# Optimization experiments

Measured on AMD Instinct MI355X. Metric: run time of the kernel, lower is better.

## Reference

```python
import jax, jax.numpy as jnp
import numpy as np

L, S, R, NUM_RESNET = 6, 2, 3, 3
N = 2 ** L            # 64 blocks per axis
NX = N * S            # 128 grid points per axis
NCART_SIDE = 80
NCART = NCART_SIDE ** 2


def _perm_idx(L_, l):
    delta = 2 ** (L_ - l - 1)
    t = np.tile(np.arange(2) * delta, delta) + np.repeat(np.arange(delta), 2)
    t = np.tile(t, 2 ** l) + np.repeat(np.arange(2 ** l) * 2 ** (L_ - l), 2 ** (L_ - l))
    return jnp.asarray(t)


def _switch_idx(L_):
    h = L_ // 2
    t = np.tile(np.arange(2 ** h) * 2 ** h, 2 ** h) + np.repeat(np.arange(2 ** h), 2 ** h)
    return jnp.asarray(t)


def _bmm2(x, g_left, g_right):
    # x: (B,p,i,q,j). Right block-diag GEMM on (q,j), then left block-diag GEMM on (p,i).
    y = jnp.einsum('bpiqj,qjk->bpiqk', x, g_right)
    return jnp.einsum('bpiqk,pio->bpoqk', y, g_left)


def _complex_layer(xr, xi, p):
    # p: stacked (r1,i1,r2,i2,r3,i3,r4,i4); complex-style cross products of the original.
    r1, i1, r2, i2, r3, i3, r4, i4 = p
    yr = _bmm2(xr, r1, r1) + _bmm2(xr, i1, i1) + _bmm2(xi, r2, i2) + _bmm2(xi, i2, r2)
    yi = _bmm2(xi, r3, r3) + _bmm2(xi, i3, i3) + _bmm2(xr, r4, i4) + _bmm2(xr, i4, r4)
    return yr, yi


def _u_layer(xr, xi, p):
    ur1, ui1, ur2, ui2, ur3, ui3, ur4, ui4 = p
    return (_bmm2(xr, ur1, ur1) + _bmm2(xr, ui2, ui2)
            + _bmm2(xi, ur3, ui3) + _bmm2(xi, ui4, ur4))


def _permute(yr, yi, idx):
    yr = jnp.take(jnp.take(yr, idx, axis=1), idx, axis=3)
    yi = jnp.take(jnp.take(yi, idx, axis=1), idx, axis=3)
    return yr, yi


def _merge(y):  # (B,N,R,N,R) -> (B,N/2,2R,N/2,2R)
    return y.reshape(y.shape[0], N // 2, 2 * R, N // 2, 2 * R)


def _split(y):  # inverse of _merge
    return y.reshape(y.shape[0], N, R, N, R)


def reference(x, Vp, Hp, Mp, Gp, Up, cart_mat, r_index):
    B = x.shape[0]
    xr = x[..., 0].reshape(B, N, S, N, S)
    xi = x[..., 1].reshape(B, N, S, N, S)
    yr, yi = _complex_layer(xr, xi, Vp)                       # (B,N,R,N,R)
    for li, l in enumerate(range(L - 1, L // 2 - 1, -1)):     # H stages (permute then merge-GEMM)
        yr, yi = _permute(yr, yi, _perm_idx(L, l))
        yr, yi = _complex_layer(_merge(yr), _merge(yi), Hp[li])
        yr, yi = _split(yr), _split(yi)
    yr, yi = _permute(yr, yi, _switch_idx(L))                 # middle switch shuffle
    for k in range(NUM_RESNET):                               # residual M blocks
        zr, zi = _complex_layer(yr, yi, Mp[k])
        yr, yi = yr + zr, yi + zi
    for li, l in enumerate(range(L // 2 - 1, -1, -1)):        # G stages (merge-GEMM then permute)
        yr, yi = _complex_layer(_merge(yr), _merge(yi), Gp[li])
        yr, yi = _split(yr), _split(yi)
        yr, yi = _permute(yr, yi, _perm_idx(L, l))
    y = _u_layer(yr, yi, Up).reshape(B, NX * NX)              # real output, (B,NX,NX) flattened
    y = jnp.take(y, r_index, axis=1)                          # polar reindexing
    out = y @ cart_mat.T                                      # polar -> cartesian interpolation
    return out.reshape(B, NCART_SIDE, NCART_SIDE)


def setup_inputs() -> dict:
    key = jax.random.key(0)
    ks = jax.random.split(key, 9)
    B = 128
    x = jax.random.normal(ks[0], (B, NX, NX, 2), dtype=jnp.float32)
    Vp = jax.random.normal(ks[1], (8, N, S, R), dtype=jnp.float32) * 0.35
    Hp = jax.random.normal(ks[2], (L // 2, 8, N // 2, 2 * R, 2 * R), dtype=jnp.float32) * 0.2
    Mp = jax.random.normal(ks[3], (NUM_RESNET, 8, N, R, R), dtype=jnp.float32) * 0.25
    Gp = jax.random.normal(ks[4], (L // 2, 8, N // 2, 2 * R, 2 * R), dtype=jnp.float32) * 0.2
    Up = jax.random.normal(ks[5], (8, N, R, S), dtype=jnp.float32) * 0.35
    cart_mat = jax.random.normal(ks[6], (NCART, NX * NX), dtype=jnp.float32) * 0.01
    r_index = jax.random.permutation(ks[7], NX * NX).astype(jnp.int32)
    return {"x": x, "Vp": Vp, "Hp": Hp, "Mp": Mp, "Gp": Gp, "Up": Up,
            "cart_mat": cart_mat, "r_index": r_index}
```

## Files before the change

### kernel.cpp

```cpp
#include <hip/hip_runtime.h>


typedef _Float16 f16;
typedef __attribute__((ext_vector_type(8))) short sx8;
typedef __attribute__((ext_vector_type(4))) float fx4;
typedef __attribute__((ext_vector_type(8))) unsigned short usx8;
typedef __attribute__((ext_vector_type(4))) unsigned short usx4;

__device__ __forceinline__ unsigned short f2bf(float f) {
  unsigned u = __builtin_bit_cast(unsigned, f);
  u = (u + 0x7FFFu + ((u >> 16) & 1u)) >> 16;
  return (unsigned short)u;
}
__device__ __forceinline__ float bf2f(unsigned short h) {
  return __builtin_bit_cast(float, ((unsigned)h) << 16);
}

template<int ID>
__device__ __forceinline__ int rp_apply(int k) {
  if constexpr (ID == 0) { return k; }
  else if constexpr (ID == 3) { return (k & 7) * 8 + (k >> 3); }
  else {
    constexpr int l = (ID == 1) ? 4 : (ID == 2) ? 3 : (ID == 4) ? 2 : (ID == 5) ? 1 : 0;
    constexpr int d = 1 << (5 - l);
    constexpr int m2 = 2 * d;
    int g = k / m2, r = k % m2;
    return g * m2 + (r & 1) * d + (r >> 1);
  }
}

__device__ __forceinline__ void term_decode(int t, int& lm, int& rm,
                                            bool& useXi, bool& toYi) {
  lm = (t < 2) ? t : (t < 4) ? (t + 4) : (t - 2);
  rm = (t >= 2 && t <= 5) ? (lm ^ 1) : lm;
  useXi = (t >= 4);
  toYi = (t >> 1) & 1;
}

#define SMEM_BYTES 36864

__device__ __forceinline__ void layer6(int g, int b, int P, int Q,
                                       const float* __restrict__ wp,
                                       const f16* ldsX, float* Y0, float* Y1,
                                       f16* __restrict__ yr,
                                       f16* __restrict__ yi) {
  int lm0, rm0, lm1, rm1;
  switch (g) {
    case 0:  lm0 = 0; rm0 = 0; lm1 = 1; rm1 = 1; break;
    case 1:  lm0 = 6; rm0 = 7; lm1 = 7; rm1 = 6; break;
    case 2:  lm0 = 2; rm0 = 3; lm1 = 3; rm1 = 2; break;
    default: lm0 = 4; rm0 = 4; lm1 = 5; rm1 = 5; break;
  }
  const int xbase = (g & 2) ? 36 : 0;
  float X[36], Y[36];
#pragma unroll
  for (int k = 0; k < 36; ++k) X[k] = (float)ldsX[(xbase + k) * 128 + b];
#pragma unroll
  for (int k = 0; k < 36; ++k) Y[k] = 0.f;

  for (int tt = 0; tt < 2; ++tt) {
    const int lm = tt ? lm1 : lm0;
    const int rm = tt ? rm1 : rm0;
    const float* Lw = wp + ((size_t)lm * 32 + P) * 36;
    const float* Rw = wp + ((size_t)rm * 32 + Q) * 36;
#pragma unroll
    for (int i = 0; i < 6; ++i) {
      float tk[6] = {0.f, 0.f, 0.f, 0.f, 0.f, 0.f};
#pragma unroll
      for (int j = 0; j < 6; ++j) {
        float xv = X[i * 6 + j];
#pragma unroll
        for (int k = 0; k < 6; ++k) tk[k] += xv * Rw[j * 6 + k];
      }
#pragma unroll
      for (int o = 0; o < 6; ++o) {
        float lv = Lw[i * 6 + o];
#pragma unroll
        for (int k = 0; k < 6; ++k) Y[o * 6 + k] += lv * tk[k];
      }
    }
  }
  __syncthreads();
  if (g == 2) {
#pragma unroll
    for (int k = 0; k < 36; ++k) Y0[k * 128 + b] = Y[k];
  } else if (g == 3) {
#pragma unroll
    for (int k = 0; k < 36; ++k) Y1[k * 128 + b] = Y[k];
  }
  __syncthreads();
  if (g == 0) {
#pragma unroll
    for (int k = 0; k < 36; ++k) {
      float v = Y[k] + Y0[k * 128 + b];
      yr[((size_t)((P * 6 + k / 6) * 192 + Q * 6 + k % 6)) * 128 + b] = (f16)v;
    }
  } else if (g == 1) {
#pragma unroll
    for (int k = 0; k < 36; ++k) {
      float v = Y[k] + Y1[k * 128 + b];
      yi[((size_t)((P * 6 + k / 6) * 192 + Q * 6 + k % 6)) * 128 + b] = (f16)v;
    }
  }
}

__global__ __launch_bounds__(256) void k_transpose(const float* __restrict__ x,
                                                   f16* __restrict__ xtr,
                                                   f16* __restrict__ xti) {
  __shared__ float ls[2][32][129];
  const int t = threadIdx.x;
  const int u = blockIdx.x;
  const int v0 = blockIdx.y * 32;
  for (int it = 0; it < 32; ++it) {
    int b = it * 4 + (t >> 6);
    int r = t & 63;
    int v = r >> 1, ch = r & 1;
    ls[ch][v][b] = x[(((size_t)b * 128 + u) * 128 + (v0 + v)) * 2 + ch];
  }
  __syncthreads();
  for (int it = 0; it < 32; ++it) {
    int idx = it * 256 + t;
    int ch = idx >> 12;
    int v = (idx >> 7) & 31;
    int b = idx & 127;
    f16* dst = ch ? xti : xtr;
    dst[((size_t)(u * 128 + v0 + v)) * 128 + b] = (f16)ls[ch][v][b];
  }
}

__global__ __launch_bounds__(512, 4) void k_vh(const f16* __restrict__ xtr,
                                               const f16* __restrict__ xti,
                                               f16* __restrict__ yr,
                                               f16* __restrict__ yi,
                                               const float* __restrict__ vp,
                                               const float* __restrict__ hp) {
  __shared__ __align__(16) char smem[SMEM_BYTES];
  f16* ldsX = (f16*)smem;
  float* Y0 = (float*)smem;
  float* Y1 = (float*)(smem + 18432);
  const int t = threadIdx.x;
  const int P = blockIdx.x, Q = blockIdx.y;
  const int g = __builtin_amdgcn_readfirstlane(t >> 7);
  const int b = t & 127;

  const int pp = g >> 1, qq = g & 1;
  const int p = 2 * P + pp, q = 2 * Q + qq;
  float Xr[4], Xi[4];
#pragma unroll
  for (int i = 0; i < 2; ++i)
#pragma unroll
    for (int j = 0; j < 2; ++j) {
      size_t off = ((size_t)((4 * P + 2 * pp + i) * 128 + (4 * Q + 2 * qq + j))) * 128 + b;
      Xr[i * 2 + j] = (float)xtr[off];
      Xi[i * 2 + j] = (float)xti[off];
    }
  float Ar[9], Ai[9];
#pragma unroll
  for (int k = 0; k < 9; ++k) { Ar[k] = 0.f; Ai[k] = 0.f; }
  for (int tt = 0; tt < 8; ++tt) {
    int lm, rm; bool useXi, toYi;
    term_decode(tt, lm, rm, useXi, toYi);
    const float* Lw = vp + ((size_t)lm * 64 + p) * 6;
    const float* Rw = vp + ((size_t)rm * 64 + q) * 6;
#pragma unroll
    for (int i = 0; i < 2; ++i) {
      float x0, x1;
      if (useXi) { x0 = Xi[i * 2 + 0]; x1 = Xi[i * 2 + 1]; }
      else       { x0 = Xr[i * 2 + 0]; x1 = Xr[i * 2 + 1]; }
      float t0 = x0 * Rw[0] + x1 * Rw[3];
      float t1 = x0 * Rw[1] + x1 * Rw[4];
      float t2 = x0 * Rw[2] + x1 * Rw[5];
      if (toYi) {
#pragma unroll
        for (int o = 0; o < 3; ++o) {
          float lv = Lw[i * 3 + o];
          Ai[o*3+0] += lv * t0; Ai[o*3+1] += lv * t1; Ai[o*3+2] += lv * t2;
        }
      } else {
#pragma unroll
        for (int o = 0; o < 3; ++o) {
          float lv = Lw[i * 3 + o];
          Ar[o*3+0] += lv * t0; Ar[o*3+1] += lv * t1; Ar[o*3+2] += lv * t2;
        }
      }
    }
  }
#pragma unroll
  for (int o = 0; o < 3; ++o)
#pragma unroll
    for (int k = 0; k < 3; ++k) {
      int ch = (3 * pp + o) * 6 + (3 * qq + k);
      ldsX[ch * 128 + b] = (f16)Ar[o * 3 + k];
      ldsX[(36 + ch) * 128 + b] = (f16)Ai[o * 3 + k];
    }
  __syncthreads();
  layer6(g, b, P, Q, hp, ldsX, Y0, Y1, yr, yi);
}

template<int PERM>
__global__ __launch_bounds__(512, 4) void k_hg(const f16* __restrict__ xr,
                                               const f16* __restrict__ xi,
                                               f16* __restrict__ yr,
                                               f16* __restrict__ yi,
                                               const float* __restrict__ wp) {
  __shared__ __align__(16) char smem[SMEM_BYTES];
  f16* ldsX = (f16*)smem;
  float* Y0 = (float*)smem;
  float* Y1 = (float*)(smem + 18432);
  const int t = threadIdx.x;
  const int P = blockIdx.x, Q = blockIdx.y;

  for (int r = 0; r < 3; ++r) {
    int idx = t + r * 512;
    if (idx < 1152) {
      int c = idx >> 4, o8 = (idx & 15) * 8;
      int cc = (c < 36) ? c : c - 36;
      int I = cc / 6, J = cc % 6;
      int grow = rp_apply<PERM>(2 * P + I / 3) * 3 + I % 3;
      int gcol = rp_apply<PERM>(2 * Q + J / 3) * 3 + J % 3;
      const f16* src = (c < 36) ? xr : xi;
      usx8 v = *(const usx8*)(src + ((size_t)(grow * 192 + gcol)) * 128 + o8);
      *(usx8*)(ldsX + c * 128 + o8) = v;
    }
  }
  __syncthreads();
  const int g = __builtin_amdgcn_readfirstlane(t >> 7);
  const int b = t & 127;
  layer6(g, b, P, Q, wp, ldsX, Y0, Y1, yr, yi);
}

__global__ __launch_bounds__(512, 4) void k_mg(const f16* __restrict__ xr,
                                               const f16* __restrict__ xi,
                                               f16* __restrict__ yr,
                                               f16* __restrict__ yi,
                                               const float* __restrict__ mp,
                                               const float* __restrict__ gp) {
  __shared__ __align__(16) char smem[SMEM_BYTES];
  f16* ldsX = (f16*)smem;
  float* Y0 = (float*)smem;
  float* Y1 = (float*)(smem + 18432);
  const int t = threadIdx.x;
  const int P = blockIdx.x, Q = blockIdx.y;
  const int g = __builtin_amdgcn_readfirstlane(t >> 7);
  const int b = t & 127;

  const int aa = g >> 1, bb = g & 1;
  const int p = 2 * P + aa, q = 2 * Q + bb;
  const int prow = rp_apply<3>(p) * 3, pcol = rp_apply<3>(q) * 3;
  float Xr[9], Xi[9];
#pragma unroll
  for (int i = 0; i < 3; ++i)
#pragma unroll
    for (int j = 0; j < 3; ++j) {
      size_t off = ((size_t)((prow + i) * 192 + (pcol + j))) * 128 + b;
      Xr[i * 3 + j] = (float)xr[off];
      Xi[i * 3 + j] = (float)xi[off];
    }
  for (int lk = 0; lk < 3; ++lk) {
    const float* wp = mp + (size_t)lk * (8 * 64 * 9);
    float Yr9[9], Yi9[9];
#pragma unroll
    for (int k = 0; k < 9; ++k) { Yr9[k] = Xr[k]; Yi9[k] = Xi[k]; }
    for (int tt = 0; tt < 8; ++tt) {
      int lm, rm; bool useXi, toYi;
      term_decode(tt, lm, rm, useXi, toYi);
      const float* Lw = wp + ((size_t)lm * 64 + p) * 9;
      const float* Rw = wp + ((size_t)rm * 64 + q) * 9;
#pragma unroll
      for (int i = 0; i < 3; ++i) {
        float x0, x1, x2;
        if (useXi) { x0 = Xi[i*3+0]; x1 = Xi[i*3+1]; x2 = Xi[i*3+2]; }
        else       { x0 = Xr[i*3+0]; x1 = Xr[i*3+1]; x2 = Xr[i*3+2]; }
        float t0 = x0 * Rw[0] + x1 * Rw[3] + x2 * Rw[6];
        float t1 = x0 * Rw[1] + x1 * Rw[4] + x2 * Rw[7];
        float t2 = x0 * Rw[2] + x1 * Rw[5] + x2 * Rw[8];
        if (toYi) {
#pragma unroll
          for (int o = 0; o < 3; ++o) {
            float lv = Lw[i * 3 + o];
            Yi9[o*3+0] += lv * t0; Yi9[o*3+1] += lv * t1; Yi9[o*3+2] += lv * t2;
          }
        } else {
#pragma unroll
          for (int o = 0; o < 3; ++o) {
            float lv = Lw[i * 3 + o];
            Yr9[o*3+0] += lv * t0; Yr9[o*3+1] += lv * t1; Yr9[o*3+2] += lv * t2;
          }
        }
      }
    }
#pragma unroll
    for (int k = 0; k < 9; ++k) { Xr[k] = Yr9[k]; Xi[k] = Yi9[k]; }
  }
#pragma unroll
  for (int i = 0; i < 3; ++i)
#pragma unroll
    for (int j = 0; j < 3; ++j) {
      int ch = (3 * aa + i) * 6 + (3 * bb + j);
      ldsX[ch * 128 + b] = (f16)Xr[i * 3 + j];
      ldsX[(36 + ch) * 128 + b] = (f16)Xi[i * 3 + j];
    }
  __syncthreads();
  layer6(g, b, P, Q, gp, ldsX, Y0, Y1, yr, yi);
}

__global__ __launch_bounds__(128, 2) void k_u(const f16* __restrict__ xr,
                                              const f16* __restrict__ xi,
                                              unsigned short* __restrict__ ut,
                                              const float* __restrict__ wp) {
  const int b = threadIdx.x;
  const int p = blockIdx.x, q = blockIdx.y;
  int rrow[3], rcol[3];
#pragma unroll
  for (int i = 0; i < 3; ++i) {
    rrow[i] = rp_apply<6>(p) * 3 + i;
    rcol[i] = rp_apply<6>(q) * 3 + i;
  }
  float X[9], Y[4] = {0.f, 0.f, 0.f, 0.f};
  auto loadX = [&](const f16* src) {
#pragma unroll
    for (int i = 0; i < 3; ++i)
#pragma unroll
      for (int j = 0; j < 3; ++j)
        X[i * 3 + j] = (float)src[((size_t)(rrow[i] * 192 + rcol[j])) * 128 + b];
  };
  auto term = [&](int lm, int rm) {
    const float* Lw = wp + ((size_t)lm * 64 + p) * 6;
    const float* Rw = wp + ((size_t)rm * 64 + q) * 6;
#pragma unroll
    for (int i = 0; i < 3; ++i) {
      float t0 = X[i*3+0] * Rw[0] + X[i*3+1] * Rw[2] + X[i*3+2] * Rw[4];
      float t1 = X[i*3+0] * Rw[1] + X[i*3+1] * Rw[3] + X[i*3+2] * Rw[5];
      Y[0] += Lw[i*2+0] * t0; Y[1] += Lw[i*2+0] * t1;
      Y[2] += Lw[i*2+1] * t0; Y[3] += Lw[i*2+1] * t1;
    }
  };
  loadX(xr); term(0, 0); term(3, 3);
  loadX(xi); term(4, 5); term(7, 6);
#pragma unroll
  for (int o = 0; o < 2; ++o)
#pragma unroll
    for (int k = 0; k < 2; ++k)
      ut[((size_t)((p * 2 + o) * 128 + (q * 2 + k))) * 128 + b] = f2bf(Y[o * 2 + k]);
}

__global__ __launch_bounds__(256) void k_gather(const unsigned short* __restrict__ ut,
                                                const int* __restrict__ r_index,
                                                unsigned short* __restrict__ yg) {
  __shared__ unsigned short ls[64][130];
  __shared__ int ridx[64];
  const int t = threadIdx.x;
  const int m0 = blockIdx.x * 64;
  if (t < 64) ridx[t] = r_index[m0 + t];
  __syncthreads();
  for (int it = 0; it < 32; ++it) {
    int idx = it * 256 + t;
    int ml = idx >> 7, b = idx & 127;
    ls[ml][b] = ut[(size_t)ridx[ml] * 128 + b];
  }
  __syncthreads();
  int b = t >> 1, half = t & 1;
#pragma unroll
  for (int c = 0; c < 4; ++c) {
    usx8 v;
#pragma unroll
    for (int e = 0; e < 8; ++e) v[e] = ls[half * 32 + c * 8 + e][b];
    *(usx8*)(yg + (size_t)b * 16384 + m0 + half * 32 + c * 8) = v;
  }
}

#define G2_KC 8
#define G2_STEPS 32
#define G2_PITCH 72

__global__ __launch_bounds__(256) void k_gemm2(const unsigned short* __restrict__ yg,
                                               const float* __restrict__ cart,
                                               unsigned short* __restrict__ partial) {
  __shared__ unsigned short As[2][128][G2_PITCH];
  __shared__ unsigned short Bs[2][64][G2_PITCH];
  const int t = threadIdx.x;
  const int lane = t & 63, w = t >> 6;
  const int kc = blockIdx.x;
  const int c0 = blockIdx.y * 64;
  const int k0 = kc * 2048;

  fx4 acc[2][4];
#pragma unroll
  for (int i = 0; i < 2; ++i)
#pragma unroll
    for (int j = 0; j < 4; ++j) acc[i][j] = (fx4)0.f;

  auto ldA = [&](int rep, int kpos) -> usx8 {
    int c = t + rep * 256;
    return *(const usx8*)(yg + (size_t)(c >> 3) * 16384 + kpos + (c & 7) * 8);
  };
  auto stA = [&](int buf, int rep, usx8 v) {
    int c = t + rep * 256;
    *(usx8*)(&As[buf][c >> 3][(c & 7) * 8]) = v;
  };
  auto ldB = [&](int rep, int kpos, fx4* f0, fx4* f1) {
    int c = t + rep * 256;
    const float* p = cart + (size_t)(c0 + (c >> 3)) * 16384 + kpos + (c & 7) * 8;
    *f0 = *(const fx4*)p;
    *f1 = *(const fx4*)(p + 4);
  };
  auto stB = [&](int buf, int rep, fx4 f0, fx4 f1) {
    int c = t + rep * 256;
    usx8 v;
    v[0]=f2bf(f0[0]); v[1]=f2bf(f0[1]); v[2]=f2bf(f0[2]); v[3]=f2bf(f0[3]);
    v[4]=f2bf(f1[0]); v[5]=f2bf(f1[1]); v[6]=f2bf(f1[2]); v[7]=f2bf(f1[3]);
    *(usx8*)(&Bs[buf][c >> 3][(c & 7) * 8]) = v;
  };

  {
    usx8 a0 = ldA(0, k0), a1 = ldA(1, k0), a2 = ldA(2, k0), a3 = ldA(3, k0);
    fx4 b00, b01, b10, b11;
    ldB(0, k0, &b00, &b01); ldB(1, k0, &b10, &b11);
    stA(0, 0, a0); stA(0, 1, a1); stA(0, 2, a2); stA(0, 3, a3);
    stB(0, 0, b00, b01); stB(0, 1, b10, b11);
  }
  __syncthreads();

  for (int s = 0; s < G2_STEPS; ++s) {
    const int cur = s & 1;
    usx8 av[4]; fx4 b00, b01, b10, b11;
    const bool pf = (s + 1 < G2_STEPS);
    if (pf) {
      int kpos = k0 + (s + 1) * 64;
      av[0] = ldA(0, kpos); av[1] = ldA(1, kpos);
      av[2] = ldA(2, kpos); av[3] = ldA(3, kpos);
      ldB(0, kpos, &b00, &b01); ldB(1, kpos, &b10, &b11);
    }
    sx8 af[2][2], bf[4][2];
#pragma unroll
    for (int mi = 0; mi < 2; ++mi)
#pragma unroll
      for (int kk = 0; kk < 2; ++kk)
        af[mi][kk] = *(const sx8*)(&As[cur][w * 32 + mi * 16 + (lane & 15)][kk * 32 + (lane >> 4) * 8]);
#pragma unroll
    for (int ni = 0; ni < 4; ++ni)
#pragma unroll
      for (int kk = 0; kk < 2; ++kk)
        bf[ni][kk] = *(const sx8*)(&Bs[cur][ni * 16 + (lane & 15)][kk * 32 + (lane >> 4) * 8]);
#pragma unroll
    for (int kk = 0; kk < 2; ++kk)
#pragma unroll
      for (int mi = 0; mi < 2; ++mi)
#pragma unroll
        for (int ni = 0; ni < 4; ++ni)
          acc[mi][ni] = __builtin_amdgcn_mfma_f32_16x16x32_bf16(af[mi][kk], bf[ni][kk], acc[mi][ni], 0, 0, 0);
    if (pf) {
      stA(cur ^ 1, 0, av[0]); stA(cur ^ 1, 1, av[1]);
      stA(cur ^ 1, 2, av[2]); stA(cur ^ 1, 3, av[3]);
      stB(cur ^ 1, 0, b00, b01); stB(cur ^ 1, 1, b10, b11);
    }
    __syncthreads();
  }

#pragma unroll
  for (int mi = 0; mi < 2; ++mi) {
    int brow = w * 32 + mi * 16 + (lane >> 4) * 4;
#pragma unroll
    for (int ni = 0; ni < 4; ++ni) {
      int cc = c0 + ni * 16 + (lane & 15);
#pragma unroll
      for (int r = 0; r < 4; ++r)
        partial[((size_t)kc * 128 + brow + r) * 6400 + cc] = f2bf(acc[mi][ni][r]);
    }
  }
}

__global__ __launch_bounds__(256) void k_reduce2(const unsigned short* __restrict__ partial,
                                                 float* __restrict__ out) {
  int i = blockIdx.x * 256 + threadIdx.x;
  fx4 s = (fx4)0.f;
#pragma unroll
  for (int kc = 0; kc < G2_KC; ++kc) {
    usx4 v = *(const usx4*)(partial + (size_t)kc * 819200 + (size_t)i * 4);
    s[0] += bf2f(v[0]); s[1] += bf2f(v[1]); s[2] += bf2f(v[2]); s[3] += bf2f(v[3]);
  }
  *(fx4*)(out + (size_t)i * 4) = s;
}

extern "C" void kernel_launch(void* const* d_in, const int* in_sizes, int n_in,
                              void* d_out, int out_size, void* d_ws, size_t ws_size,
                              hipStream_t stream) {
  const float* x    = (const float*)d_in[0];
  const float* Vp   = (const float*)d_in[1];
  const float* Hp   = (const float*)d_in[2];
  const float* Mp   = (const float*)d_in[3];
  const float* Gp   = (const float*)d_in[4];
  const float* Up   = (const float*)d_in[5];
  const float* cart = (const float*)d_in[6];
  const int*   ridx = (const int*)d_in[7];
  float* out = (float*)d_out;
  unsigned short* hb = (unsigned short*)d_ws;

  const size_t PSZ = 4718592;
  f16* P0r = (f16*)(hb);
  f16* P0i = (f16*)(hb + PSZ);
  f16* P1r = (f16*)(hb + 2 * PSZ);
  f16* P1i = (f16*)(hb + 3 * PSZ);
  f16* xtr = (f16*)(hb + 4 * PSZ);
  f16* xti = (f16*)(hb + 4 * PSZ + 2097152);
  unsigned short* ut = hb + 4 * PSZ;
  unsigned short* yg = hb + 4 * PSZ + 2097152;
  unsigned short* partial = hb;

  const size_t HSZ = 8 * 32 * 36;

  k_transpose<<<dim3(128, 4), 256, 0, stream>>>(x, xtr, xti);
  k_vh<<<dim3(32, 32), 512, 0, stream>>>(xtr, xti, P0r, P0i, Vp, Hp + 0 * HSZ);
  k_hg<1><<<dim3(32, 32), 512, 0, stream>>>(P0r, P0i, P1r, P1i, Hp + 1 * HSZ);
  k_hg<2><<<dim3(32, 32), 512, 0, stream>>>(P1r, P1i, P0r, P0i, Hp + 2 * HSZ);
  k_mg<<<dim3(32, 32), 512, 0, stream>>>(P0r, P0i, P1r, P1i, Mp, Gp + 0 * HSZ);
  k_hg<4><<<dim3(32, 32), 512, 0, stream>>>(P1r, P1i, P0r, P0i, Gp + 1 * HSZ);
  k_hg<5><<<dim3(32, 32), 512, 0, stream>>>(P0r, P0i, P1r, P1i, Gp + 2 * HSZ);
  k_u<<<dim3(64, 64), 128, 0, stream>>>(P1r, P1i, ut, Up);
  k_gather<<<dim3(256), 256, 0, stream>>>(ut, ridx, yg);
  k_gemm2<<<dim3(G2_KC, 100), 256, 0, stream>>>(yg, cart, partial);
  k_reduce2<<<dim3(800), 256, 0, stream>>>(partial, out);
  (void)in_sizes; (void)n_in; (void)out_size; (void)ws_size;
}
```

Measured before the change: 300.1 us.

## Recast butterfly layers as per-block dense 72x72 operators applied with MFMA

Each H/G layer block is rewritten so the Kronecker-product weights (left and right, complex cross terms) are expanded in LDS into a dense 72x72 fp16 operator. That operator is then applied to the 72x128 batch tile with 16x16x32 f16 MFMA instructions instead of scalar FMA loops. The V layer and the three M resnet layers are also folded algebraically into the following H or G operator, so each fused kernel does one MFMA GEMM. The cost is building dense operators per block and extra fp16 rounding of the combined weights.

```diff
diff --git a/kernel.cpp b/kernel.cpp
--- a/kernel.cpp
+++ b/kernel.cpp
@@ -2,6 +2,7 @@
 
 
 typedef _Float16 f16;
+typedef __attribute__((ext_vector_type(8))) _Float16 hx8;
 typedef __attribute__((ext_vector_type(8))) short sx8;
 typedef __attribute__((ext_vector_type(4))) float fx4;
 typedef __attribute__((ext_vector_type(8))) unsigned short usx8;
@@ -29,79 +30,58 @@
   }
 }
 
-__device__ __forceinline__ void term_decode(int t, int& lm, int& rm,
-                                            bool& useXi, bool& toYi) {
-  lm = (t < 2) ? t : (t < 4) ? (t + 4) : (t - 2);
-  rm = (t >= 2 && t <= 5) ? (lm ^ 1) : lm;
-  useXi = (t >= 4);
-  toYi = (t >> 1) & 1;
-}
-
-#define SMEM_BYTES 36864
-
-__device__ __forceinline__ void layer6(int g, int b, int P, int Q,
-                                       const float* __restrict__ wp,
-                                       const f16* ldsX, float* Y0, float* Y1,
-                                       f16* __restrict__ yr,
-                                       f16* __restrict__ yi) {
-  int lm0, rm0, lm1, rm1;
-  switch (g) {
-    case 0:  lm0 = 0; rm0 = 0; lm1 = 1; rm1 = 1; break;
-    case 1:  lm0 = 6; rm0 = 7; lm1 = 7; rm1 = 6; break;
-    case 2:  lm0 = 2; rm0 = 3; lm1 = 3; rm1 = 2; break;
-    default: lm0 = 4; rm0 = 4; lm1 = 5; rm1 = 5; break;
-  }
-  const int xbase = (g & 2) ? 36 : 0;
-  float X[36], Y[36];
-#pragma unroll
-  for (int k = 0; k < 36; ++k) X[k] = (float)ldsX[(xbase + k) * 128 + b];
-#pragma unroll
-  for (int k = 0; k < 36; ++k) Y[k] = 0.f;
-
-  for (int tt = 0; tt < 2; ++tt) {
-    const int lm = tt ? lm1 : lm0;
-    const int rm = tt ? rm1 : rm0;
-    const float* Lw = wp + ((size_t)lm * 32 + P) * 36;
-    const float* Rw = wp + ((size_t)rm * 32 + Q) * 36;
-#pragma unroll
-    for (int i = 0; i < 6; ++i) {
-      float tk[6] = {0.f, 0.f, 0.f, 0.f, 0.f, 0.f};
-#pragma unroll
-      for (int j = 0; j < 6; ++j) {
-        float xv = X[i * 6 + j];
-#pragma unroll
-        for (int k = 0; k < 6; ++k) tk[k] += xv * Rw[j * 6 + k];
+__device__ __forceinline__ void qterm(int co, int ci, int tt, int& lm, int& rm) {
+  if (!co && !ci) { lm = tt;     rm = tt;     }
+  else if (!co)   { lm = 2 + tt; rm = 3 - tt; }
+  else if (!ci)   { lm = 6 + tt; rm = 7 - tt; }
+  else            { lm = 4 + tt; rm = 4 + tt; }
+}
+
+template<int NKC, int GP>
+__device__ __forceinline__ void lay_mfma(const f16* Gl, const f16* Xl,
+                                         int P, int Q, int t,
+                                         f16* __restrict__ yr,
+                                         f16* __restrict__ yi) {
+  const int w = t >> 6, lane = t & 63;
+  const int lrow = lane & 15, lgr = lane >> 4;
+  fx4 acc[5][2];
+#pragma unroll
+  for (int mt = 0; mt < 5; ++mt) { acc[mt][0] = (fx4)0.f; acc[mt][1] = (fx4)0.f; }
+#pragma unroll
+  for (int kc = 0; kc < NKC; ++kc) {
+    hx8 af[5], bf[2];
+#pragma unroll
+    for (int mt = 0; mt < 5; ++mt)
+      af[mt] = *(const hx8*)(Gl + (mt * 16 + lrow) * GP + kc * 32 + lgr * 8);
+#pragma unroll
+    for (int nt2 = 0; nt2 < 2; ++nt2) {
+      int n = (2 * w + nt2) * 16 + lrow;
+      int k0 = kc * 32 + lgr * 8;
+      hx8 b;
+#pragma unroll
+      for (int j = 0; j < 8; ++j) b[j] = Xl[(k0 + j) * 136 + n];
+      bf[nt2] = b;
+    }
+#pragma unroll
+    for (int mt = 0; mt < 5; ++mt)
+#pragma unroll
+      for (int nt2 = 0; nt2 < 2; ++nt2)
+        acc[mt][nt2] = __builtin_amdgcn_mfma_f32_16x16x32_f16(af[mt], bf[nt2], acc[mt][nt2], 0, 0, 0);
+  }
+#pragma unroll
+  for (int mt = 0; mt < 5; ++mt)
+#pragma unroll
+    for (int nt2 = 0; nt2 < 2; ++nt2)
+#pragma unroll
+      for (int r = 0; r < 4; ++r) {
+        int row = mt * 16 + lgr * 4 + r;
+        if (row >= 72) continue;
+        int n = (2 * w + nt2) * 16 + lrow;
+        int c = row >= 36;
+        int s = row - c * 36;
+        size_t off = ((size_t)((P * 6 + s / 6) * 192 + (Q * 6 + s % 6))) * 128 + n;
+        (c ? yi : yr)[off] = (f16)acc[mt][nt2][r];
       }
-#pragma unroll
-      for (int o = 0; o < 6; ++o) {
-        float lv = Lw[i * 6 + o];
-#pragma unroll
-        for (int k = 0; k < 6; ++k) Y[o * 6 + k] += lv * tk[k];
-      }
-    }
-  }
-  __syncthreads();
-  if (g == 2) {
-#pragma unroll
-    for (int k = 0; k < 36; ++k) Y0[k * 128 + b] = Y[k];
-  } else if (g == 3) {
-#pragma unroll
-    for (int k = 0; k < 36; ++k) Y1[k * 128 + b] = Y[k];
-  }
-  __syncthreads();
-  if (g == 0) {
-#pragma unroll
-    for (int k = 0; k < 36; ++k) {
-      float v = Y[k] + Y0[k * 128 + b];
-      yr[((size_t)((P * 6 + k / 6) * 192 + Q * 6 + k % 6)) * 128 + b] = (f16)v;
-    }
-  } else if (g == 1) {
-#pragma unroll
-    for (int k = 0; k < 36; ++k) {
-      float v = Y[k] + Y1[k * 128 + b];
-      yi[((size_t)((P * 6 + k / 6) * 192 + Q * 6 + k % 6)) * 128 + b] = (f16)v;
-    }
-  }
 }
 
 __global__ __launch_bounds__(256) void k_transpose(const float* __restrict__ x,
@@ -128,180 +108,236 @@
   }
 }
 
-__global__ __launch_bounds__(512, 4) void k_vh(const f16* __restrict__ xtr,
-                                               const f16* __restrict__ xti,
-                                               f16* __restrict__ yr,
-                                               f16* __restrict__ yi,
-                                               const float* __restrict__ vp,
-                                               const float* __restrict__ hp) {
-  __shared__ __align__(16) char smem[SMEM_BYTES];
-  f16* ldsX = (f16*)smem;
-  float* Y0 = (float*)smem;
-  float* Y1 = (float*)(smem + 18432);
+template<int PERM>
+__global__ __launch_bounds__(256) void k_lay(const f16* __restrict__ xr,
+                                             const f16* __restrict__ xi,
+                                             f16* __restrict__ yr,
+                                             f16* __restrict__ yi,
+                                             const float* __restrict__ wp) {
+  __shared__ float Wl[8][36], Wr[8][36];
+  __shared__ __align__(16) f16 Gl[80 * 104];
+  __shared__ __align__(16) f16 Xl[96 * 136];
   const int t = threadIdx.x;
   const int P = blockIdx.x, Q = blockIdx.y;
-  const int g = __builtin_amdgcn_readfirstlane(t >> 7);
-  const int b = t & 127;
-
-  const int pp = g >> 1, qq = g & 1;
-  const int p = 2 * P + pp, q = 2 * Q + qq;
-  float Xr[4], Xi[4];
-#pragma unroll
-  for (int i = 0; i < 2; ++i)
-#pragma unroll
-    for (int j = 0; j < 2; ++j) {
-      size_t off = ((size_t)((4 * P + 2 * pp + i) * 128 + (4 * Q + 2 * qq + j))) * 128 + b;
-      Xr[i * 2 + j] = (float)xtr[off];
-      Xi[i * 2 + j] = (float)xti[off];
-    }
-  float Ar[9], Ai[9];
-#pragma unroll
-  for (int k = 0; k < 9; ++k) { Ar[k] = 0.f; Ai[k] = 0.f; }
-  for (int tt = 0; tt < 8; ++tt) {
-    int lm, rm; bool useXi, toYi;
-    term_decode(tt, lm, rm, useXi, toYi);
-    const float* Lw = vp + ((size_t)lm * 64 + p) * 6;
-    const float* Rw = vp + ((size_t)rm * 64 + q) * 6;
-#pragma unroll
-    for (int i = 0; i < 2; ++i) {
-      float x0, x1;
-      if (useXi) { x0 = Xi[i * 2 + 0]; x1 = Xi[i * 2 + 1]; }
-      else       { x0 = Xr[i * 2 + 0]; x1 = Xr[i * 2 + 1]; }
-      float t0 = x0 * Rw[0] + x1 * Rw[3];
-      float t1 = x0 * Rw[1] + x1 * Rw[4];
-      float t2 = x0 * Rw[2] + x1 * Rw[5];
-      if (toYi) {
-#pragma unroll
-        for (int o = 0; o < 3; ++o) {
-          float lv = Lw[i * 3 + o];
-          Ai[o*3+0] += lv * t0; Ai[o*3+1] += lv * t1; Ai[o*3+2] += lv * t2;
-        }
-      } else {
-#pragma unroll
-        for (int o = 0; o < 3; ++o) {
-          float lv = Lw[i * 3 + o];
-          Ar[o*3+0] += lv * t0; Ar[o*3+1] += lv * t1; Ar[o*3+2] += lv * t2;
-        }
-      }
-    }
-  }
-#pragma unroll
-  for (int o = 0; o < 3; ++o)
-#pragma unroll
-    for (int k = 0; k < 3; ++k) {
-      int ch = (3 * pp + o) * 6 + (3 * qq + k);
-      ldsX[ch * 128 + b] = (f16)Ar[o * 3 + k];
-      ldsX[(36 + ch) * 128 + b] = (f16)Ai[o * 3 + k];
-    }
-  __syncthreads();
-  layer6(g, b, P, Q, hp, ldsX, Y0, Y1, yr, yi);
-}
-
-template<int PERM>
-__global__ __launch_bounds__(512, 4) void k_hg(const f16* __restrict__ xr,
-                                               const f16* __restrict__ xi,
-                                               f16* __restrict__ yr,
-                                               f16* __restrict__ yi,
-                                               const float* __restrict__ wp) {
-  __shared__ __align__(16) char smem[SMEM_BYTES];
-  f16* ldsX = (f16*)smem;
-  float* Y0 = (float*)smem;
-  float* Y1 = (float*)(smem + 18432);
+  for (int idx = t; idx < 288; idx += 256) {
+    int lm = idx / 36, e = idx % 36;
+    Wl[lm][e] = wp[((size_t)lm * 32 + P) * 36 + e];
+    Wr[lm][e] = wp[((size_t)lm * 32 + Q) * 36 + e];
+  }
+  __syncthreads();
+  for (int idx = t; idx < 80 * 104; idx += 256) {
+    int u = idx / 104, v = idx % 104;
+    float g = 0.f;
+    if (u < 72 && v < 72) {
+      int co = u / 36, ru = u % 36, O = ru / 6, K2 = ru % 6;
+      int ci = v / 36, sv = v % 36, I = sv / 6, J = sv % 6;
+      int lm0, rm0, lm1, rm1;
+      qterm(co, ci, 0, lm0, rm0);
+      qterm(co, ci, 1, lm1, rm1);
+      g = Wl[lm0][I * 6 + O] * Wr[rm0][J * 6 + K2]
+        + Wl[lm1][I * 6 + O] * Wr[rm1][J * 6 + K2];
+    }
+    Gl[idx] = (f16)g;
+  }
+  for (int idx = t; idx < 96 * 16; idx += 256) {
+    int row = idx / 16, seg = idx % 16;
+    usx8 v = (usx8)((unsigned short)0);
+    if (row < 72) {
+      int c = row / 36, sv = row % 36, I = sv / 6, J = sv % 6;
+      int grow = rp_apply<PERM>(2 * P + I / 3) * 3 + I % 3;
+      int gcol = rp_apply<PERM>(2 * Q + J / 3) * 3 + J % 3;
+      const unsigned short* src = (const unsigned short*)(c ? xi : xr);
+      v = *(const usx8*)(src + (size_t)(grow * 192 + gcol) * 128 + seg * 8);
+    }
+    *(usx8*)((unsigned short*)Xl + row * 136 + seg * 8) = v;
+  }
+  __syncthreads();
+  lay_mfma<3, 104>(Gl, Xl, P, Q, t, yr, yi);
+}
+
+__global__ __launch_bounds__(256) void k_vhm(const f16* __restrict__ xtr,
+                                             const f16* __restrict__ xti,
+                                             f16* __restrict__ yr,
+                                             f16* __restrict__ yi,
+                                             const float* __restrict__ vp,
+                                             const float* __restrict__ hp) {
+  __shared__ float Wl[8][36], Wr[8][36];
+  __shared__ float Vl[8][2][6], Vr[8][2][6];
+  __shared__ float H72[72 * 72];
+  __shared__ float Vq[4][18][8];
+  __shared__ __align__(16) f16 Gv[80 * 40];
+  __shared__ __align__(16) f16 Xv[32 * 136];
   const int t = threadIdx.x;
   const int P = blockIdx.x, Q = blockIdx.y;
-
-  for (int r = 0; r < 3; ++r) {
-    int idx = t + r * 512;
-    if (idx < 1152) {
-      int c = idx >> 4, o8 = (idx & 15) * 8;
-      int cc = (c < 36) ? c : c - 36;
-      int I = cc / 6, J = cc % 6;
-      int grow = rp_apply<PERM>(2 * P + I / 3) * 3 + I % 3;
-      int gcol = rp_apply<PERM>(2 * Q + J / 3) * 3 + J % 3;
-      const f16* src = (c < 36) ? xr : xi;
-      usx8 v = *(const usx8*)(src + ((size_t)(grow * 192 + gcol)) * 128 + o8);
-      *(usx8*)(ldsX + c * 128 + o8) = v;
-    }
-  }
-  __syncthreads();
-  const int g = __builtin_amdgcn_readfirstlane(t >> 7);
-  const int b = t & 127;
-  layer6(g, b, P, Q, wp, ldsX, Y0, Y1, yr, yi);
-}
-
-__global__ __launch_bounds__(512, 4) void k_mg(const f16* __restrict__ xr,
-                                               const f16* __restrict__ xi,
-                                               f16* __restrict__ yr,
-                                               f16* __restrict__ yi,
-                                               const float* __restrict__ mp,
-                                               const float* __restrict__ gp) {
-  __shared__ __align__(16) char smem[SMEM_BYTES];
-  f16* ldsX = (f16*)smem;
-  float* Y0 = (float*)smem;
-  float* Y1 = (float*)(smem + 18432);
+  for (int idx = t; idx < 288; idx += 256) {
+    int lm = idx / 36, e = idx % 36;
+    Wl[lm][e] = hp[((size_t)lm * 32 + P) * 36 + e];
+    Wr[lm][e] = hp[((size_t)lm * 32 + Q) * 36 + e];
+  }
+  for (int idx = t; idx < 96; idx += 256) {
+    int lm = idx / 12, r = idx % 12, aa = r / 6, e = r % 6;
+    Vl[lm][aa][e] = vp[((size_t)lm * 64 + (2 * P + aa)) * 6 + e];
+    Vr[lm][aa][e] = vp[((size_t)lm * 64 + (2 * Q + aa)) * 6 + e];
+  }
+  __syncthreads();
+  for (int idx = t; idx < 72 * 72; idx += 256) {
+    int u = idx / 72, v = idx % 72;
+    int co = u / 36, ru = u % 36, O = ru / 6, K2 = ru % 6;
+    int ci = v / 36, sv = v % 36, I = sv / 6, J = sv % 6;
+    int lm0, rm0, lm1, rm1;
+    qterm(co, ci, 0, lm0, rm0);
+    qterm(co, ci, 1, lm1, rm1);
+    H72[idx] = Wl[lm0][I * 6 + O] * Wr[rm0][J * 6 + K2]
+             + Wl[lm1][I * 6 + O] * Wr[rm1][J * 6 + K2];
+  }
+  for (int idx = t; idx < 4 * 18 * 8; idx += 256) {
+    int s = idx / 144, r = idx % 144, a = r / 8, b = r % 8;
+    int ca = a / 9, ra = a % 9, o = ra / 3, k3 = ra % 3;
+    int cb = b >> 2, i2 = (b >> 1) & 1, j2 = b & 1;
+    int aa = s >> 1, bb = s & 1;
+    int lm0, rm0, lm1, rm1;
+    qterm(ca, cb, 0, lm0, rm0);
+    qterm(ca, cb, 1, lm1, rm1);
+    Vq[s][a][b] = Vl[lm0][aa][i2 * 3 + o] * Vr[rm0][bb][j2 * 3 + k3]
+                + Vl[lm1][aa][i2 * 3 + o] * Vr[rm1][bb][j2 * 3 + k3];
+  }
+  __syncthreads();
+  for (int idx = t; idx < 80 * 40; idx += 256) {
+    int u = idx / 40, v = idx % 40;
+    float g = 0.f;
+    if (u < 72 && v < 32) {
+      int s = v >> 3, aa = s >> 1, bb = s & 1;
+      int c = (v >> 2) & 1, i2 = (v >> 1) & 1, j2 = v & 1;
+#pragma unroll
+      for (int cw = 0; cw < 2; ++cw)
+#pragma unroll
+        for (int o = 0; o < 3; ++o)
+#pragma unroll
+          for (int k3 = 0; k3 < 3; ++k3)
+            g += H72[u * 72 + cw * 36 + (3 * aa + o) * 6 + (3 * bb + k3)]
+               * Vq[s][cw * 9 + o * 3 + k3][c * 4 + i2 * 2 + j2];
+    }
+    Gv[idx] = (f16)g;
+  }
+  for (int idx = t; idx < 32 * 16; idx += 256) {
+    int row = idx / 16, seg = idx % 16;
+    int s = row >> 3, aa = s >> 1, bb = s & 1;
+    int c = (row >> 2) & 1, i2 = (row >> 1) & 1, j2 = row & 1;
+    const unsigned short* src = (const unsigned short*)(c ? xti : xtr);
+    usx8 v = *(const usx8*)(src + (size_t)((4 * P + 2 * aa + i2) * 128 + (4 * Q + 2 * bb + j2)) * 128 + seg * 8);
+    *(usx8*)((unsigned short*)Xv + row * 136 + seg * 8) = v;
+  }
+  __syncthreads();
+  lay_mfma<1, 40>(Gv, Xv, P, Q, t, yr, yi);
+}
+
+__global__ __launch_bounds__(256) void k_mgm(const f16* __restrict__ xr,
+                                             const f16* __restrict__ xi,
+                                             f16* __restrict__ yr,
+                                             f16* __restrict__ yi,
+                                             const float* __restrict__ mp,
+                                             const float* __restrict__ gp) {
+  __shared__ __align__(16) char sm[58688];
+  float (*Ml)[8][2][9] = (float (*)[8][2][9])(sm + 0);
+  float (*Mr)[8][2][9] = (float (*)[8][2][9])(sm + 1728);
+  float (*Wl)[36]      = (float (*)[36])(sm + 3456);
+  float (*Wr)[36]      = (float (*)[36])(sm + 4608);
+  float (*C)[18][18]   = (float (*)[18][18])(sm + 5760);
+  float (*T)[18][18]   = (float (*)[18][18])(sm + 10944);
+  float (*D)[18][18]   = (float (*)[18][18])(sm + 16128);
+  float* G1            = (float*)(sm + 21312);
+  f16*   Gm            = (f16*)(sm + 42048);
+  f16*   Xm            = (f16*)(sm + 0);
   const int t = threadIdx.x;
   const int P = blockIdx.x, Q = blockIdx.y;
-  const int g = __builtin_amdgcn_readfirstlane(t >> 7);
-  const int b = t & 127;
-
-  const int aa = g >> 1, bb = g & 1;
-  const int p = 2 * P + aa, q = 2 * Q + bb;
-  const int prow = rp_apply<3>(p) * 3, pcol = rp_apply<3>(q) * 3;
-  float Xr[9], Xi[9];
-#pragma unroll
-  for (int i = 0; i < 3; ++i)
-#pragma unroll
-    for (int j = 0; j < 3; ++j) {
-      size_t off = ((size_t)((prow + i) * 192 + (pcol + j))) * 128 + b;
-      Xr[i * 3 + j] = (float)xr[off];
-      Xi[i * 3 + j] = (float)xi[off];
-    }
-  for (int lk = 0; lk < 3; ++lk) {
-    const float* wp = mp + (size_t)lk * (8 * 64 * 9);
-    float Yr9[9], Yi9[9];
-#pragma unroll
-    for (int k = 0; k < 9; ++k) { Yr9[k] = Xr[k]; Yi9[k] = Xi[k]; }
-    for (int tt = 0; tt < 8; ++tt) {
-      int lm, rm; bool useXi, toYi;
-      term_decode(tt, lm, rm, useXi, toYi);
-      const float* Lw = wp + ((size_t)lm * 64 + p) * 9;
-      const float* Rw = wp + ((size_t)rm * 64 + q) * 9;
-#pragma unroll
-      for (int i = 0; i < 3; ++i) {
-        float x0, x1, x2;
-        if (useXi) { x0 = Xi[i*3+0]; x1 = Xi[i*3+1]; x2 = Xi[i*3+2]; }
-        else       { x0 = Xr[i*3+0]; x1 = Xr[i*3+1]; x2 = Xr[i*3+2]; }
-        float t0 = x0 * Rw[0] + x1 * Rw[3] + x2 * Rw[6];
-        float t1 = x0 * Rw[1] + x1 * Rw[4] + x2 * Rw[7];
-        float t2 = x0 * Rw[2] + x1 * Rw[5] + x2 * Rw[8];
-        if (toYi) {
-#pragma unroll
-          for (int o = 0; o < 3; ++o) {
-            float lv = Lw[i * 3 + o];
-            Yi9[o*3+0] += lv * t0; Yi9[o*3+1] += lv * t1; Yi9[o*3+2] += lv * t2;
-          }
-        } else {
-#pragma unroll
-          for (int o = 0; o < 3; ++o) {
-            float lv = Lw[i * 3 + o];
-            Yr9[o*3+0] += lv * t0; Yr9[o*3+1] += lv * t1; Yr9[o*3+2] += lv * t2;
-          }
-        }
-      }
-    }
-#pragma unroll
-    for (int k = 0; k < 9; ++k) { Xr[k] = Yr9[k]; Xi[k] = Yi9[k]; }
-  }
-#pragma unroll
-  for (int i = 0; i < 3; ++i)
-#pragma unroll
-    for (int j = 0; j < 3; ++j) {
-      int ch = (3 * aa + i) * 6 + (3 * bb + j);
-      ldsX[ch * 128 + b] = (f16)Xr[i * 3 + j];
-      ldsX[(36 + ch) * 128 + b] = (f16)Xi[i * 3 + j];
-    }
-  __syncthreads();
-  layer6(g, b, P, Q, gp, ldsX, Y0, Y1, yr, yi);
+
+  for (int idx = t; idx < 432; idx += 256) {
+    int lk = idx / 144, r0 = idx % 144, lm = r0 / 18, r1 = r0 % 18, aa = r1 / 9, e = r1 % 9;
+    Ml[lk][lm][aa][e] = mp[(((size_t)lk * 8 + lm) * 64 + (2 * P + aa)) * 9 + e];
+    Mr[lk][lm][aa][e] = mp[(((size_t)lk * 8 + lm) * 64 + (2 * Q + aa)) * 9 + e];
+  }
+  for (int idx = t; idx < 288; idx += 256) {
+    int lm = idx / 36, e = idx % 36;
+    Wl[lm][e] = gp[((size_t)lm * 32 + P) * 36 + e];
+    Wr[lm][e] = gp[((size_t)lm * 32 + Q) * 36 + e];
+  }
+  __syncthreads();
+  auto buildIM = [&](int lk, float (*OUT)[18][18]) {
+    for (int idx = t; idx < 4 * 324; idx += 256) {
+      int s = idx / 324, r = idx % 324, a = r / 18, b = r % 18;
+      int ca = a / 9, ra = a % 9, o = ra / 3, k3 = ra % 3;
+      int cb = b / 9, rb = b % 9, i = rb / 3, j = rb % 3;
+      int aa = s >> 1, bb = s & 1;
+      int lm0, rm0, lm1, rm1;
+      qterm(ca, cb, 0, lm0, rm0);
+      qterm(ca, cb, 1, lm1, rm1);
+      float val = Ml[lk][lm0][aa][i * 3 + o] * Mr[lk][rm0][bb][j * 3 + k3]
+                + Ml[lk][lm1][aa][i * 3 + o] * Mr[lk][rm1][bb][j * 3 + k3];
+      if (a == b) val += 1.f;
+      OUT[s][a][b] = val;
+    }
+  };
+  auto matmul18 = [&](float (*OUT)[18][18], float (*A)[18][18], float (*B)[18][18]) {
+    for (int idx = t; idx < 4 * 324; idx += 256) {
+      int s = idx / 324, r = idx % 324, a = r / 18, b = r % 18;
+      float acc = 0.f;
+#pragma unroll
+      for (int c18 = 0; c18 < 18; ++c18) acc += A[s][a][c18] * B[s][c18][b];
+      OUT[s][a][b] = acc;
+    }
+  };
+  buildIM(0, C);
+  buildIM(1, T);
+  for (int idx = t; idx < 72 * 72; idx += 256) {
+    int u = idx / 72, v = idx % 72;
+    int co = u / 36, ru = u % 36, O = ru / 6, K2 = ru % 6;
+    int ci = v / 36, sv = v % 36, I = sv / 6, J = sv % 6;
+    int lm0, rm0, lm1, rm1;
+    qterm(co, ci, 0, lm0, rm0);
+    qterm(co, ci, 1, lm1, rm1);
+    G1[idx] = Wl[lm0][I * 6 + O] * Wr[rm0][J * 6 + K2]
+            + Wl[lm1][I * 6 + O] * Wr[rm1][J * 6 + K2];
+  }
+  __syncthreads();
+  matmul18(D, T, C);
+  __syncthreads();
+  buildIM(2, T);
+  __syncthreads();
+  matmul18(C, T, D);
+  __syncthreads();
+  for (int idx = t; idx < 80 * 104; idx += 256) {
+    int u = idx / 104, v = idx % 104;
+    float g = 0.f;
+    if (u < 72 && v < 72) {
+      int cv = v / 36, sv = v % 36, I = sv / 6, J = sv % 6;
+      int aa = I / 3, bb = J / 3, i = I % 3, j = J % 3;
+      int s = aa * 2 + bb, v18 = cv * 9 + i * 3 + j;
+#pragma unroll
+      for (int cw = 0; cw < 2; ++cw)
+#pragma unroll
+        for (int i2 = 0; i2 < 3; ++i2)
+#pragma unroll
+          for (int j2 = 0; j2 < 3; ++j2)
+            g += G1[u * 72 + cw * 36 + (3 * aa + i2) * 6 + (3 * bb + j2)]
+               * C[s][cw * 9 + i2 * 3 + j2][v18];
+    }
+    Gm[idx] = (f16)g;
+  }
+  __syncthreads();
+  for (int idx = t; idx < 96 * 16; idx += 256) {
+    int row = idx / 16, seg = idx % 16;
+    usx8 v = (usx8)((unsigned short)0);
+    if (row < 72) {
+      int c = row / 36, sv = row % 36, I = sv / 6, J = sv % 6;
+      int grow = rp_apply<3>(2 * P + I / 3) * 3 + I % 3;
+      int gcol = rp_apply<3>(2 * Q + J / 3) * 3 + J % 3;
+      const unsigned short* src = (const unsigned short*)(c ? xi : xr);
+      v = *(const usx8*)(src + (size_t)(grow * 192 + gcol) * 128 + seg * 8);
+    }
+    *(usx8*)((unsigned short*)Xm + row * 136 + seg * 8) = v;
+  }
+  __syncthreads();
+  lay_mfma<3, 104>(Gm, Xm, P, Q, t, yr, yi);
 }
 
 __global__ __launch_bounds__(128, 2) void k_u(const f16* __restrict__ xr,
@@ -510,12 +546,12 @@
   const size_t HSZ = 8 * 32 * 36;
 
   k_transpose<<<dim3(128, 4), 256, 0, stream>>>(x, xtr, xti);
-  k_vh<<<dim3(32, 32), 512, 0, stream>>>(xtr, xti, P0r, P0i, Vp, Hp + 0 * HSZ);
-  k_hg<1><<<dim3(32, 32), 512, 0, stream>>>(P0r, P0i, P1r, P1i, Hp + 1 * HSZ);
-  k_hg<2><<<dim3(32, 32), 512, 0, stream>>>(P1r, P1i, P0r, P0i, Hp + 2 * HSZ);
-  k_mg<<<dim3(32, 32), 512, 0, stream>>>(P0r, P0i, P1r, P1i, Mp, Gp + 0 * HSZ);
-  k_hg<4><<<dim3(32, 32), 512, 0, stream>>>(P1r, P1i, P0r, P0i, Gp + 1 * HSZ);
-  k_hg<5><<<dim3(32, 32), 512, 0, stream>>>(P0r, P0i, P1r, P1i, Gp + 2 * HSZ);
+  k_vhm<<<dim3(32, 32), 256, 0, stream>>>(xtr, xti, P0r, P0i, Vp, Hp + 0 * HSZ);
+  k_lay<1><<<dim3(32, 32), 256, 0, stream>>>(P0r, P0i, P1r, P1i, Hp + 1 * HSZ);
+  k_lay<2><<<dim3(32, 32), 256, 0, stream>>>(P1r, P1i, P0r, P0i, Hp + 2 * HSZ);
+  k_mgm<<<dim3(32, 32), 256, 0, stream>>>(P0r, P0i, P1r, P1i, Mp, Gp + 0 * HSZ);
+  k_lay<4><<<dim3(32, 32), 256, 0, stream>>>(P1r, P1i, P0r, P0i, Gp + 1 * HSZ);
+  k_lay<5><<<dim3(32, 32), 256, 0, stream>>>(P0r, P0i, P1r, P1i, Gp + 2 * HSZ);
   k_u<<<dim3(64, 64), 128, 0, stream>>>(P1r, P1i, ut, Up);
   k_gather<<<dim3(256), 256, 0, stream>>>(ut, ridx, yg);
   k_gemm2<<<dim3(G2_KC, 100), 256, 0, stream>>>(yg, cart, partial);
```

Result: slower. 342.1 us (+14.0%).
